# Performance work log

Hardware: AMD Instinct MI355X
Metric: run time of the kernel (lower is better)

## Reference

```python
import jax, jax.numpy as jnp
import numpy as np
from jax import lax

C = 31  # channels (hyperspectral bands)
DN = ('NCHW', 'OIHW', 'NCHW')


def ln_bias(x, w, b):
    # WithBias LayerNorm over channel dim (torch does it in (b,hw,c) layout)
    mu = x.mean(axis=1, keepdims=True)
    var = x.var(axis=1, keepdims=True)
    xn = (x - mu) * lax.rsqrt(var + 1e-5)
    return xn * w[None, :, None, None] + b[None, :, None, None]


def conv1x1(x, W, b):
    y = lax.conv_general_dilated(x, W, (1, 1), 'VALID', dimension_numbers=DN)
    return y + b[None, :, None, None]


def dwconv3(x, W, b=None):
    c = x.shape[1]
    y = lax.conv_general_dilated(x, W, (1, 1), ((1, 1), (1, 1)),
                                 dimension_numbers=DN, feature_group_count=c)
    if b is not None:
        y = y + b[None, :, None, None]
    return y


def l2norm_lastdim(v):
    n = jnp.sqrt(jnp.sum(v * v, axis=-1, keepdims=True))
    return v / jnp.maximum(n, 1e-12)


def setup_inputs() -> dict:
    key = jax.random.key(0)
    ks = jax.random.split(key, 16)
    B, H, W = 4, 512, 512
    s = 0.05
    d = {
        'x': jax.random.normal(ks[0], (B, 1, H, W), jnp.float32),
        'z': jax.random.normal(ks[1], (B, C, H, W), jnp.float32),
        'nx_w': jnp.ones((1,), jnp.float32),
        'nx_b': jnp.zeros((1,), jnp.float32),
        'nz_w': jnp.ones((C,), jnp.float32),
        'nz_b': jnp.zeros((C,), jnp.float32),
        't1_w': jax.random.normal(ks[2], (C, C, 1, 1), jnp.float32) * s,
        't1_b': jnp.zeros((C,), jnp.float32),
        't2_w': jax.random.normal(ks[3], (C, 1, 3, 3), jnp.float32) * s,
        't2_b': jnp.zeros((C,), jnp.float32),
        'p1_w': jax.random.normal(ks[4], (C, 1, 1, 1), jnp.float32) * s,
        'p1_b': jnp.zeros((C,), jnp.float32),
        'p2_w': jax.random.normal(ks[5], (C, 1, 3, 3), jnp.float32) * s,
        'p2_b': jnp.zeros((C,), jnp.float32),
        'g1_w': jax.random.normal(ks[6], (C, C, 1, 1), jnp.float32) * s,
        'g1_b': jnp.zeros((C,), jnp.float32),
        'g2_w': jax.random.normal(ks[7], (C, 1, 3, 3), jnp.float32) * s,
        'g2_b': jnp.zeros((C,), jnp.float32),
        'w_w': jax.random.normal(ks[8], (C, C, 1, 1), jnp.float32) * s,
        'w_b': jnp.zeros((C,), jnp.float32),
        'v_w': jax.random.normal(ks[9], (C + 1, C + 1, 1, 1), jnp.float32) * s,
        'v_b': jnp.zeros((C + 1,), jnp.float32),
        'pe1_w': jax.random.normal(ks[10], (C, 1, 3, 3), jnp.float32) * s,
        'pe2_w': jax.random.normal(ks[11], (C, 1, 3, 3), jnp.float32) * s,
    }
    return d


def reference(x, z, nx_w, nx_b, nz_w, nz_b, t1_w, t1_b, t2_w, t2_b,
              p1_w, p1_b, p2_w, p2_b, g1_w, g1_b, g2_w, g2_b,
              w_w, w_b, v_w, v_b, pe1_w, pe2_w):
    b, _, h, w = x.shape
    x0 = ln_bias(x, nx_w, nx_b)            # (b,1,h,w)
    z0 = ln_bias(z, nz_w, nz_b)            # (b,C,h,w)

    z1 = dwconv3(conv1x1(z0, t1_w, t1_b), t2_w, t2_b).reshape(b, C, h * w)
    x1 = dwconv3(conv1x1(x0, p1_w, p1_b), p2_w, p2_b).reshape(b, C, h * w)

    z1 = l2norm_lastdim(z1)
    x1 = l2norm_lastdim(x1)

    att = jax.nn.softmax(jnp.einsum('bcn,bdn->bcd', z1, x1), axis=-1)  # (b,C,C)

    z2 = dwconv3(conv1x1(z0, g1_w, g1_b), g2_w, g2_b)  # (b,C,h,w)
    z_v = z2.reshape(b, C, h * w)
    out_x = jnp.einsum('bcd,bdn->bcn', att, z_v).reshape(b, C, h, w)

    pos = dwconv3(jax.nn.gelu(dwconv3(z2, pe1_w), approximate=False), pe2_w)
    out_x = conv1x1(out_x, w_w, w_b) + pos + z

    y = conv1x1(jnp.concatenate([x, out_x], axis=1), v_w, v_b)  # (b,C+1,h,w)
    return y
```

## Files before the change

kernel.cpp:

```cpp
#include <hip/hip_runtime.h>
#include <hip/hip_fp16.h>
#include <math.h>

#define BN 4
#define CC 31
#define HH 512
#define WW 512
#define HWSZ 262144

static const size_t Z2F = (size_t)BN * CC * HWSZ;
#define T_OFF   0
#define SSQ_OFF 124
#define R0_OFF  248
#define RL_OFF  372
#define C0_OFF  496
#define CL_OFF  620
#define COR_OFF 744
#define M2_OFF  1240
#define VB2_OFF 5208

typedef short v8s __attribute__((ext_vector_type(8)));
typedef _Float16 v8h __attribute__((ext_vector_type(8)));
typedef float v4f __attribute__((ext_vector_type(4)));
typedef _Float16 v4h __attribute__((ext_vector_type(4)));

__device__ __forceinline__ short f2bf(float f) {
    unsigned u = __float_as_uint(f);
    return (short)((u + 0x7FFFu + ((u >> 16) & 1u)) >> 16);
}

__device__ __forceinline__ float fast_gelu(float s) {
    const float a  = fabsf(s) * 0.70710678118654752f;
    const float t  = __builtin_amdgcn_rcpf(1.f + 0.3275911f * a);
    float p = 1.061405429f;
    p = p * t - 1.453152027f;
    p = p * t + 1.421413741f;
    p = p * t - 0.284496736f;
    p = p * t + 0.254829592f;
    const float e  = __expf(-a * a);
    const float er = copysignf(1.f - p * t * e, s);
    return 0.5f * s * (1.f + er);
}

__device__ __forceinline__ void swizzle_tile(int& b, int& ty0, int& tx0) {
    const int lid = blockIdx.x + 32 * blockIdx.y + 1024 * blockIdx.z;
    const int vid = ((lid & 7) << 9) + (lid >> 3);
    b = vid >> 10;
    const int rem = vid & 1023;
    ty0 = (rem >> 5) << 4;
    tx0 = (rem & 31) << 4;
}

__global__ __launch_bounds__(256, 4) void blockNL_k_stage1(
    const float* __restrict__ z,
    const float* __restrict__ nz_w, const float* __restrict__ nz_b,
    const float* __restrict__ t1w, const float* __restrict__ t1b,
    const float* __restrict__ t2w, const float* __restrict__ t2b,
    const float* __restrict__ g1w, const float* __restrict__ g1b,
    const float* __restrict__ g2w, const float* __restrict__ g2b,
    __half* __restrict__ z2out, float* __restrict__ stats)
{
    __shared__ __align__(16) short Vb[324 * 32];
    __shared__ __align__(16) short Wp[16 * 32];
    __shared__ __align__(16) union {
        short Ff[324 * 16];
        short Zb[16 * 264];
    } uf;
    __shared__ __align__(16) short Wd[10 * 16];

    const int tid = threadIdx.x;
    int b, ty0, tx0;
    swizzle_tile(b, ty0, tx0);

    const int w = tid >> 6, lane = tid & 63, quad = lane >> 4, m15 = lane & 15;
    const int ty = tid >> 4, tx = tid & 15;
    const int gy = ty0 + ty, gx = tx0 + tx;

    for (int hp = tid; hp < 324; hp += 256) {
        const int hy = hp / 18, hx = hp - hy * 18;
        const int zy = ty0 + hy - 1, zx = tx0 + hx - 1;
        const bool valid = ((unsigned)zy < (unsigned)HH) && ((unsigned)zx < (unsigned)WW);
        int pk[16];
        if (valid) {
            const float* zp = z + (size_t)b * CC * HWSZ + (size_t)zy * WW + zx;
            float v[CC];
            float mu = 0.f;
            #pragma unroll
            for (int c = 0; c < CC; ++c) { v[c] = zp[(size_t)c * HWSZ]; mu += v[c]; }
            mu *= (1.f / 31.f);
            float var = 0.f;
            #pragma unroll
            for (int c = 0; c < CC; ++c) { float d = v[c] - mu; v[c] = d; var += d * d; }
            var *= (1.f / 31.f);
            const float rs = rsqrtf(var + 1e-5f);
            #pragma unroll
            for (int c = 0; c < CC; ++c) v[c] = v[c] * rs * nz_w[c] + nz_b[c];
            #pragma unroll
            for (int i = 0; i < 15; ++i)
                asm("v_cvt_pk_bf16_f32 %0, %1, %2"
                    : "=v"(pk[i]) : "v"(v[2 * i]), "v"(v[2 * i + 1]));
            asm("v_cvt_pk_bf16_f32 %0, %1, %2"
                : "=v"(pk[15]) : "v"(v[30]), "v"(0.f));
        } else {
            #pragma unroll
            for (int i = 0; i < 16; ++i) pk[i] = 0;
        }
        int* dst = (int*)&Vb[hp * 32];
        #pragma unroll
        for (int q = 0; q < 4; ++q) {
            int4 t; t.x = pk[q*4]; t.y = pk[q*4+1]; t.z = pk[q*4+2]; t.w = pk[q*4+3];
            ((int4*)dst)[q] = t;
        }
    }

    auto wbuild = [&](int p) {
        const float* W1 = (p >= 2) ? g1w : t1w;
        const int ct = p & 1;
        const int m = tid >> 4, kp = tid & 15;
        const int gr = ct * 16 + m;
        const int k0 = 2 * kp, k1 = k0 + 1;
        float w0 = 0.f, w1 = 0.f;
        if (gr < CC) {
            if (k0 < CC) w0 = W1[gr * CC + k0];
            if (k1 < CC) w1 = W1[gr * CC + k1];
        }
        ((int*)Wp)[m * 16 + kp] =
            (int)((unsigned short)f2bf(w0) | ((unsigned)(unsigned short)f2bf(w1) << 16));
    };

    auto wdbuild = [&](int p) {
        if (tid < 160) {
            const float* W3 = (p >= 2) ? g2w : t2w;
            const float* B3 = (p >= 2) ? g2b : t2b;
            const int tap = tid >> 4, r = tid & 15;
            const int ch = (p & 1) * 16 + r;
            float v = 0.f;
            if (ch < CC) v = (tap < 9) ? W3[ch * 9 + tap] : B3[ch];
            Wd[tap * 16 + r] = (short)__half_as_ushort(__float2half(v));
        }
    };

    auto mfma_pass = [&](int p) {
        const int ct = p & 1;
        const float* B1 = (p >= 2) ? g1b : t1b;
        const v8s afrag = *(const v8s*)&Wp[m15 * 32 + quad * 8];
        float bias[4];
        #pragma unroll
        for (int r = 0; r < 4; ++r) {
            const int row = ct * 16 + quad * 4 + r;
            bias[r] = (row < CC) ? B1[row] : 0.f;
        }
        for (int j = w; j < 21; j += 4) {
            const int px = j * 16 + m15;
            const int pc = (px < 324) ? px : 323;
            const v8s bfrag = *(const v8s*)&Vb[pc * 32 + quad * 8];
            v4f acc = {0.f, 0.f, 0.f, 0.f};
            acc = __builtin_amdgcn_mfma_f32_16x16x32_bf16(afrag, bfrag, acc, 0, 0, 0);
            if (px < 324) {
                unsigned d0 = (unsigned)__half_as_ushort(__float2half(acc[0] + bias[0]))
                            | ((unsigned)__half_as_ushort(__float2half(acc[1] + bias[1])) << 16);
                unsigned d1 = (unsigned)__half_as_ushort(__float2half(acc[2] + bias[2]))
                            | ((unsigned)__half_as_ushort(__float2half(acc[3] + bias[3])) << 16);
                const int half = (quad >> 1) ^ ((px >> 2) & 1);
                int2 st; st.x = (int)d0; st.y = (int)d1;
                *(int2*)&uf.Ff[px * 16 + half * 8 + (quad & 1) * 4] = st;
            }
        }
    };

    auto dw3_compute = [&](__half2* accv) {
        {
            const v8s b0 = *(const v8s*)&Wd[9 * 16 + 0];
            const v8s b1 = *(const v8s*)&Wd[9 * 16 + 8];
            #pragma unroll
            for (int i = 0; i < 4; ++i) {
                accv[i]     = ((const __half2*)&b0)[i];
                accv[4 + i] = ((const __half2*)&b1)[i];
            }
        }
        #pragma unroll
        for (int dy = 0; dy < 3; ++dy)
            #pragma unroll
            for (int dx = 0; dx < 3; ++dx) {
                const int tap = dy * 3 + dx;
                const int hp = (ty + dy) * 18 + (tx + dx);
                const int sel = (hp >> 2) & 1;
                const v8s f0 = *(const v8s*)&uf.Ff[hp * 16 + sel * 8];
                const v8s f1 = *(const v8s*)&uf.Ff[hp * 16 + (sel ^ 1) * 8];
                const v8s w0 = *(const v8s*)&Wd[tap * 16 + 0];
                const v8s w1 = *(const v8s*)&Wd[tap * 16 + 8];
                #pragma unroll
                for (int i = 0; i < 4; ++i) {
                    accv[i]     = __hfma2(((const __half2*)&w0)[i],
                                          ((const __half2*)&f0)[i], accv[i]);
                    accv[4 + i] = __hfma2(((const __half2*)&w1)[i],
                                          ((const __half2*)&f1)[i], accv[4 + i]);
                }
            }
    };

    auto dw3_writeT = [&](int ct, const __half2* accv) {
        #pragma unroll
        for (int i = 0; i < 8; ++i) {
            const unsigned u = *(const unsigned*)&accv[i];
            uf.Zb[(2 * i) * 264 + tid]     = (short)(u & 0xFFFFu);
            uf.Zb[(2 * i + 1) * 264 + tid] = (short)(u >> 16);
        }
        const bool top = (gy == 0), bot = (gy == HH - 1);
        const bool lef = (gx == 0), rig = (gx == WW - 1);
        if (top | bot | lef | rig) {
            #pragma unroll
            for (int r = 0; r < 16; ++r) {
                const int ch = ct * 16 + r;
                if (ch < CC) {
                    const unsigned u = *(const unsigned*)&accv[r >> 1];
                    const float sT = __half2float(__ushort_as_half(
                        (unsigned short)((r & 1) ? (u >> 16) : (u & 0xFFFFu))));
                    if (top) atomicAdd(&stats[R0_OFF + b * CC + ch], sT);
                    if (bot) atomicAdd(&stats[RL_OFF + b * CC + ch], sT);
                    if (lef) atomicAdd(&stats[C0_OFF + b * CC + ch], sT);
                    if (rig) atomicAdd(&stats[CL_OFF + b * CC + ch], sT);
                    if ((top || bot) && (lef || rig))
                        stats[COR_OFF + (b * CC + ch) * 4 +
                              (bot ? 2 : 0) + (rig ? 1 : 0)] = sT;
                }
            }
        }
    };

    auto dw3_writeG = [&](int ct, const __half2* accv) {
        const size_t zbase = (size_t)b * CC * HWSZ + (size_t)gy * WW + gx;
        #pragma unroll
        for (int i = 0; i < 8; ++i) {
            const unsigned u = *(const unsigned*)&accv[i];
            const int ch0 = ct * 16 + 2 * i, ch1 = ch0 + 1;
            z2out[zbase + (size_t)ch0 * HWSZ] =
                __ushort_as_half((unsigned short)(u & 0xFFFFu));
            if (ch1 < CC)
                z2out[zbase + (size_t)ch1 * HWSZ] =
                    __ushort_as_half((unsigned short)(u >> 16));
        }
    };

    auto stats_pass = [&](int ct) {
        const bool dosq = (w >> 1);
        const int kh = w & 1;
        v8h onesh;
        #pragma unroll
        for (int i = 0; i < 8; ++i) onesh[i] = (_Float16)1.f;
        v4f acc = {0.f, 0.f, 0.f, 0.f};
        #pragma unroll
        for (int i = 0; i < 4; ++i) {
            const int ks = kh * 4 + i;
            const v8h bf = *(const v8h*)&uf.Zb[m15 * 264 + ks * 32 + quad * 8];
            acc = __builtin_amdgcn_mfma_f32_16x16x32_f16(dosq ? bf : onesh, bf, acc, 0, 0, 0);
        }
        if (!dosq) {
            if (quad == 0) {
                const int ch = ct * 16 + m15;
                if (ch < CC) atomicAdd(&stats[T_OFF + b * CC + ch], acc[0]);
            }
        } else {
            if ((m15 >> 2) == quad) {
                const int r = m15 & 3;
                const int ch = ct * 16 + m15;
                if (ch < CC) atomicAdd(&stats[SSQ_OFF + b * CC + ch], acc[r]);
            }
        }
    };

    __half2 accv[8];

    wbuild(0); wdbuild(0);
    __syncthreads();
    mfma_pass(0);
    __syncthreads();
    dw3_compute(accv);
    __syncthreads();
    dw3_writeT(0, accv);
    __syncthreads();
    stats_pass(0); wbuild(1); wdbuild(1);
    __syncthreads();
    mfma_pass(1);
    __syncthreads();
    dw3_compute(accv);
    __syncthreads();
    dw3_writeT(1, accv);
    __syncthreads();
    stats_pass(1); wbuild(2); wdbuild(2);
    __syncthreads();
    mfma_pass(2);
    __syncthreads();
    dw3_compute(accv); dw3_writeG(2, accv); wbuild(3);
    __syncthreads();
    mfma_pass(3); wdbuild(3);
    __syncthreads();
    dw3_compute(accv); dw3_writeG(3, accv);
}

__global__ void blockNL_k_att(
    const float* __restrict__ nx_b,
    const float* __restrict__ p1w, const float* __restrict__ p1b,
    const float* __restrict__ p2w, const float* __restrict__ p2b,
    const float* __restrict__ ww,  const float* __restrict__ wb,
    const float* __restrict__ vw,  const float* __restrict__ vb,
    float* stats)
{
    __shared__ float x1v[CC][9];
    __shared__ float dxs[CC];
    __shared__ float att[CC][CC];
    __shared__ float WA[CC][CC];

    const int tid = threadIdx.x;
    const int b = blockIdx.x;
    const float cnt[9] = {1.f, 510.f, 1.f, 510.f, 260100.f, 510.f, 1.f, 510.f, 1.f};

    if (tid < CC) {
        const float a = nx_b[0];
        const float u = p1w[tid] * a + p1b[tid];
        float w9[9];
        #pragma unroll
        for (int k = 0; k < 9; ++k) w9[k] = p2w[tid * 9 + k];
        float ssq = 0.f;
        #pragma unroll
        for (int ry = 0; ry < 3; ++ry) {
            #pragma unroll
            for (int rx = 0; rx < 3; ++rx) {
                float wsum = 0.f;
                #pragma unroll
                for (int ky = 0; ky < 3; ++ky) {
                    #pragma unroll
                    for (int kx = 0; kx < 3; ++kx) {
                        const bool okr = (ry == 1) || (ry == 0 && ky >= 1) || (ry == 2 && ky <= 1);
                        const bool okc = (rx == 1) || (rx == 0 && kx >= 1) || (rx == 2 && kx <= 1);
                        if (okr && okc) wsum += w9[ky * 3 + kx];
                    }
                }
                const float val = u * wsum + p2b[tid];
                x1v[tid][ry * 3 + rx] = val;
                ssq += cnt[ry * 3 + rx] * val * val;
            }
        }
        dxs[tid] = fmaxf(sqrtf(ssq), 1e-12f);
    }
    if (b == 0 && tid < 32) {
        float s = vb[tid];
        #pragma unroll
        for (int c = 0; c < CC; ++c) s += vw[tid * 32 + c + 1] * wb[c];
        stats[VB2_OFF + tid] = s;
    }
    __syncthreads();

    if (tid < CC) {
        const int c = tid;
        const float Tt  = stats[T_OFF  + b * CC + c];
        const float sq  = stats[SSQ_OFF + b * CC + c];
        const float r0  = stats[R0_OFF + b * CC + c];
        const float rL  = stats[RL_OFF + b * CC + c];
        const float c0  = stats[C0_OFF + b * CC + c];
        const float cL  = stats[CL_OFF + b * CC + c];
        const float k00 = stats[COR_OFF + (b * CC + c) * 4 + 0];
        const float k01 = stats[COR_OFF + (b * CC + c) * 4 + 1];
        const float k10 = stats[COR_OFF + (b * CC + c) * 4 + 2];
        const float k11 = stats[COR_OFF + (b * CC + c) * 4 + 3];
        float T[9];
        T[0] = k00; T[2] = k01; T[6] = k10; T[8] = k11;
        T[1] = r0 - k00 - k01;
        T[7] = rL - k10 - k11;
        T[3] = c0 - k00 - k10;
        T[5] = cL - k01 - k11;
        T[4] = Tt - r0 - rL - c0 - cL + k00 + k01 + k10 + k11;
        const float dz = fmaxf(sqrtf(sq), 1e-12f);

        float Arow[CC];
        float mx = -3.4e38f;
        #pragma unroll
        for (int d = 0; d < CC; ++d) {
            float s = 0.f;
            #pragma unroll
            for (int r = 0; r < 9; ++r) s += T[r] * x1v[d][r];
            s = s / (dz * dxs[d]);
            Arow[d] = s;
            mx = fmaxf(mx, s);
        }
        float den = 0.f;
        #pragma unroll
        for (int d = 0; d < CC; ++d) { float e = expf(Arow[d] - mx); Arow[d] = e; den += e; }
        const float inv = 1.f / den;
        #pragma unroll
        for (int d = 0; d < CC; ++d) att[c][d] = Arow[d] * inv;
    }
    __syncthreads();
    if (tid < CC) {
        const int c2 = tid;
        #pragma unroll
        for (int d = 0; d < CC; ++d) {
            float s = 0.f;
            #pragma unroll
            for (int c = 0; c < CC; ++c) s += ww[c2 * CC + c] * att[c][d];
            WA[c2][d] = s;
        }
    }
    __syncthreads();
    if (tid < 32) {
        const int e = tid;
        #pragma unroll
        for (int d = 0; d < CC; ++d) {
            float s = 0.f;
            #pragma unroll
            for (int c2 = 0; c2 < CC; ++c2) s += vw[e * 32 + c2 + 1] * WA[c2][d];
            stats[M2_OFF + (b * 32 + e) * CC + d] = s;
        }
    }
}

__global__ __launch_bounds__(256, 4) void blockNL_k_out(
    const float* __restrict__ x, const float* __restrict__ z,
    const float* __restrict__ vw,
    const float* __restrict__ pe1w, const float* __restrict__ pe2w,
    const __half* __restrict__ z2, const float* __restrict__ stats,
    float* __restrict__ out)
{
    __shared__ __align__(16) unsigned zb2[4][400];
    __shared__ __align__(16) unsigned qb2[4][324];
    __shared__ __align__(16) short Ub[256 * 20];
    __shared__ __align__(16) short A2[4 * 32 * 20];
    __shared__ unsigned W1h[144];
    __shared__ unsigned W2h[144];

    const int tid = threadIdx.x;
    int b, ty0, tx0;
    swizzle_tile(b, ty0, tx0);
    const int ty = tid >> 4, tx = tid & 15;
    const int gy = ty0 + ty, gx = tx0 + tx;

    const float* M2 = stats + M2_OFF + b * 32 * CC;
    for (int idx = tid; idx < 2048; idx += 256) {
        const int ci = idx >> 9, e = (idx >> 4) & 31, k = idx & 15;
        const int ch = ci * 8 + (k & 7);
        float v = 0.f;
        if (ch < 31) v = (k < 8) ? vw[e * 32 + 1 + ch] : M2[e * CC + ch];
        A2[(ci * 32 + e) * 20 + k] = (short)__half_as_ushort(__float2half(v));
    }
    for (int idx = tid; idx < 288; idx += 256) {
        const int t = (idx >= 144);
        const int r = idx - t * 144;
        const int ci = r / 36, rem = r - ci * 36;
        const int tap = rem >> 2, pr = rem & 3;
        const int ch0 = ci * 8 + 2 * pr, ch1 = ch0 + 1;
        const float* Ws = t ? pe2w : pe1w;
        const float a = Ws[ch0 * 9 + tap];
        const float bb = (ch1 < 31) ? Ws[ch1 * 9 + tap] : 0.f;
        const unsigned u = (unsigned)__half_as_ushort(__float2half(a))
                         | ((unsigned)__half_as_ushort(__float2half(bb)) << 16);
        (t ? W2h : W1h)[r] = u;
    }

    const int w = tid >> 6, lane = tid & 63, quad = lane >> 4, m15 = lane & 15;
    const int mt = w & 1, jbase = (w >> 1) * 8;
    const size_t zpix = (size_t)b * CC * HWSZ + (size_t)gy * WW + gx;

    int  gzo[6];
    bool gvv[6];
    #pragma unroll
    for (int k = 0; k < 6; ++k) {
        const int p = lane + 64 * k;
        const int hy = p / 18, hx = p - hy * 18;
        const bool inr = (p < 324);
        gzo[k] = inr ? (hy * 20 + hx) : 0;
        gvv[k] = inr && ((unsigned)(ty0 + hy - 1) < (unsigned)HH) &&
                 ((unsigned)(tx0 + hx - 1) < (unsigned)WW);
    }
    const bool sact = (tid < 200);
    const int shy = tid / 10, shx2 = (tid - shy * 10) * 2;
    const int szy = ty0 + shy - 2, szx = tx0 + shx2 - 2;
    const bool sv = sact && ((unsigned)szy < (unsigned)HH) &&
                    ((unsigned)szx < (unsigned)WW);
    const long sgoff = (long)szy * WW + szx;
    const int zwo = shy * 20 + shx2;

    v4f acc[8];
    #pragma unroll
    for (int jj = 0; jj < 8; ++jj) acc[jj] = (v4f){0.f, 0.f, 0.f, 0.f};

    auto stage = [&](int ci) {
        const unsigned short* z2u = (const unsigned short*)z2;
        #pragma unroll
        for (int pr = 0; pr < 4; ++pr) {
            const int ch0 = ci * 8 + 2 * pr, ch1 = ch0 + 1;
            unsigned wa = 0, wb = 0;
            if (sv) {
                wa = *(const unsigned*)(z2u + (size_t)(b * CC + ch0) * HWSZ + sgoff);
                if (ch1 < 31)
                    wb = *(const unsigned*)(z2u + (size_t)(b * CC + ch1) * HWSZ + sgoff);
            }
            const unsigned u0 = (wa & 0xFFFFu) | (wb << 16);
            const unsigned u1 = (wa >> 16) | (wb & 0xFFFF0000u);
            if (sact) {
                uint2 st; st.x = u0; st.y = u1;
                *(uint2*)&zb2[pr][zwo] = st;
            }
        }
    };

    stage(0);

    for (int ci = 0; ci < 4; ++ci) {
        __syncthreads();
        {
            const int pr = w;
            unsigned wv2[9];
            #pragma unroll
            for (int t = 0; t < 9; ++t) wv2[t] = W1h[ci * 36 + t * 4 + pr];
            #pragma unroll
            for (int k = 0; k < 6; ++k) {
                const int p = lane + 64 * k;
                if (k < 5 || p < 324) {
                    unsigned qo = 0;
                    if (gvv[k]) {
                        __half2 s2h = __float2half2_rn(0.f);
                        #pragma unroll
                        for (int dy = 0; dy < 3; ++dy)
                            #pragma unroll
                            for (int dx = 0; dx < 3; ++dx)
                                s2h = __hfma2(*(const __half2*)&wv2[dy * 3 + dx],
                                              *(const __half2*)&zb2[pr][gzo[k] + dy * 20 + dx],
                                              s2h);
                        const float2 f = __half22float2(s2h);
                        const float q0 = fast_gelu(f.x), q1 = fast_gelu(f.y);
                        qo = (unsigned)__half_as_ushort(__float2half(q0))
                           | ((unsigned)__half_as_ushort(__float2half(q1)) << 16);
                    }
                    qb2[pr][p] = qo;
                }
            }
        }
        __syncthreads();
        {
            __half2 pos2[4];
            #pragma unroll
            for (int pr = 0; pr < 4; ++pr) pos2[pr] = __float2half2_rn(0.f);
            #pragma unroll
            for (int dy = 0; dy < 3; ++dy)
                #pragma unroll
                for (int dx = 0; dx < 3; ++dx) {
                    const int tap = dy * 3 + dx;
                    const int qoff = (ty + dy) * 18 + (tx + dx);
                    #pragma unroll
                    for (int pr = 0; pr < 4; ++pr) {
                        const unsigned wq = W2h[ci * 36 + tap * 4 + pr];
                        pos2[pr] = __hfma2(*(const __half2*)&wq,
                                           *(const __half2*)&qb2[pr][qoff], pos2[pr]);
                    }
                }
            unsigned tpk[4], zc[4];
            const int ctr = (ty + 2) * 20 + (tx + 2);
            #pragma unroll
            for (int pr = 0; pr < 4; ++pr) {
                zc[pr] = zb2[pr][ctr];
                const int ch0 = ci * 8 + 2 * pr, ch1 = ch0 + 1;
                const float2 pf = __half22float2(pos2[pr]);
                const float t0 = pf.x + z[zpix + (size_t)ch0 * HWSZ];
                float t1 = 0.f;
                if (ch1 < 31) t1 = pf.y + z[zpix + (size_t)ch1 * HWSZ];
                tpk[pr] = (unsigned)__half_as_ushort(__float2half(t0))
                        | ((unsigned)__half_as_ushort(__float2half(t1)) << 16);
            }
            int* ub = (int*)&Ub[tid * 20];
            int2 s0, s1, s2, s3;
            s0.x = (int)tpk[0]; s0.y = (int)tpk[1];
            s1.x = (int)tpk[2]; s1.y = (int)tpk[3];
            s2.x = (int)zc[0];  s2.y = (int)zc[1];
            s3.x = (int)zc[2];  s3.y = (int)zc[3];
            ((int2*)ub)[0] = s0;
            ((int2*)ub)[1] = s1;
            ((int2*)ub)[2] = s2;
            ((int2*)ub)[3] = s3;
        }
        __syncthreads();
        {
            const v4h a = *(const v4h*)&A2[(ci * 32 + mt * 16 + m15) * 20 + quad * 4];
            #pragma unroll
            for (int jj = 0; jj < 8; ++jj) {
                const int p = (jbase + jj) * 16 + m15;
                const v4h bv = *(const v4h*)&Ub[p * 20 + quad * 4];
                acc[jj] = __builtin_amdgcn_mfma_f32_16x16x16f16(a, bv, acc[jj], 0, 0, 0);
            }
        }
        if (ci < 3) stage(ci + 1);
    }

    {
        float vb2r[4], vw0[4];
        #pragma unroll
        for (int r = 0; r < 4; ++r) {
            const int e = mt * 16 + quad * 4 + r;
            vb2r[r] = stats[VB2_OFF + e];
            vw0[r]  = vw[e * 32];
        }
        #pragma unroll
        for (int jj = 0; jj < 8; ++jj) {
            const int p = (jbase + jj) * 16 + m15;
            const int py = p >> 4, px = p & 15;
            const int ogy = ty0 + py, ogx = tx0 + px;
            const float xv = x[(size_t)b * HWSZ + (size_t)ogy * WW + ogx];
            const size_t obase = (size_t)b * 32 * HWSZ + (size_t)ogy * WW + ogx;
            #pragma unroll
            for (int r = 0; r < 4; ++r) {
                const int e = mt * 16 + quad * 4 + r;
                out[obase + (size_t)e * HWSZ] = acc[jj][r] + vb2r[r] + vw0[r] * xv;
            }
        }
    }
}

extern "C" void kernel_launch(void* const* d_in, const int* in_sizes, int n_in,
                              void* d_out, int out_size, void* d_ws, size_t ws_size,
                              hipStream_t stream)
{
    (void)in_sizes; (void)n_in; (void)out_size; (void)ws_size;

    const float* x    = (const float*)d_in[0];
    const float* z    = (const float*)d_in[1];
    const float* nx_b = (const float*)d_in[3];
    const float* nz_w = (const float*)d_in[4];
    const float* nz_b = (const float*)d_in[5];
    const float* t1w  = (const float*)d_in[6];
    const float* t1b  = (const float*)d_in[7];
    const float* t2w  = (const float*)d_in[8];
    const float* t2b  = (const float*)d_in[9];
    const float* p1w  = (const float*)d_in[10];
    const float* p1b  = (const float*)d_in[11];
    const float* p2w  = (const float*)d_in[12];
    const float* p2b  = (const float*)d_in[13];
    const float* g1w  = (const float*)d_in[14];
    const float* g1b  = (const float*)d_in[15];
    const float* g2w  = (const float*)d_in[16];
    const float* g2b  = (const float*)d_in[17];
    const float* ww   = (const float*)d_in[18];
    const float* wb   = (const float*)d_in[19];
    const float* vw   = (const float*)d_in[20];
    const float* vb   = (const float*)d_in[21];
    const float* pe1w = (const float*)d_in[22];
    const float* pe2w = (const float*)d_in[23];

    __half* z2   = (__half*)d_ws;
    float* stats = (float*)((char*)d_ws + Z2F * sizeof(__half));

    hipMemsetAsync(stats, 0, 1240 * sizeof(float), stream);

    dim3 grid(WW / 16, HH / 16, BN);
    dim3 blk(256);

    blockNL_k_stage1<<<grid, blk, 0, stream>>>(z, nz_w, nz_b, t1w, t1b, t2w, t2b,
                                               g1w, g1b, g2w, g2b, z2, stats);
    blockNL_k_att<<<4, 64, 0, stream>>>(nx_b, p1w, p1b, p2w, p2b, ww, wb, vw, vb,
                                        stats);
    blockNL_k_out<<<grid, blk, 0, stream>>>(x, z, vw, pe1w, pe2w, z2, stats,
                                            (float*)d_out);
}
```

Measured before the change: 573.3 us.

## Fuse attention-matrix kernel into output kernel, recomputing per block

Removes the separate tiny attention kernel launch (4 blocks of 64 threads) by having every output block recompute the 31x31 softmax attention, the W·att and V·(W·att) products, and the bias fold from the global stats. The results go straight into the fp16 A2 MFMA operand in shared memory, and the shared buffers for this step are unioned with the halo buffers. This removes one kernel launch and the serialization bubble between kernels. In exchange, 4096 blocks each redo roughly 60K FMAs of small matrix work plus extra barriers, and the added registers may affect occupancy.

```diff
diff --git a/kernel.cpp b/kernel.cpp
--- a/kernel.cpp
+++ b/kernel.cpp
@@ -16,8 +16,6 @@
 #define C0_OFF  496
 #define CL_OFF  620
 #define COR_OFF 744
-#define M2_OFF  1240
-#define VB2_OFF 5208
 
 typedef short v8s __attribute__((ext_vector_type(8)));
 typedef _Float16 v8h __attribute__((ext_vector_type(8)));
@@ -298,59 +296,100 @@
     dw3_compute(accv); dw3_writeG(3, accv);
 }
 
-__global__ void blockNL_k_att(
+__global__ __launch_bounds__(256, 4) void blockNL_k_out(
+    const float* __restrict__ x, const float* __restrict__ z,
     const float* __restrict__ nx_b,
     const float* __restrict__ p1w, const float* __restrict__ p1b,
     const float* __restrict__ p2w, const float* __restrict__ p2b,
     const float* __restrict__ ww,  const float* __restrict__ wb,
     const float* __restrict__ vw,  const float* __restrict__ vb,
-    float* stats)
+    const float* __restrict__ pe1w, const float* __restrict__ pe2w,
+    const __half* __restrict__ z2, const float* __restrict__ stats,
+    float* __restrict__ out)
 {
-    __shared__ float x1v[CC][9];
-    __shared__ float dxs[CC];
-    __shared__ float att[CC][CC];
-    __shared__ float WA[CC][CC];
+    __shared__ __align__(16) union {
+        struct {
+            unsigned zb2[4][400];
+            unsigned qb2[4][324];
+        } s;
+        struct {
+            float x1v[CC][9];
+            float dxs[CC];
+            float att[CC][CC];
+            float WA[CC][CC];
+        } a;
+    } uu;
+    __shared__ __align__(16) short Ub[256 * 20];
+    __shared__ __align__(16) short A2[4 * 32 * 20];
+    __shared__ unsigned W1h[144];
+    __shared__ unsigned W2h[144];
+    __shared__ float vb2s[32];
 
     const int tid = threadIdx.x;
-    const int b = blockIdx.x;
-    const float cnt[9] = {1.f, 510.f, 1.f, 510.f, 260100.f, 510.f, 1.f, 510.f, 1.f};
-
-    if (tid < CC) {
-        const float a = nx_b[0];
-        const float u = p1w[tid] * a + p1b[tid];
-        float w9[9];
-        #pragma unroll
-        for (int k = 0; k < 9; ++k) w9[k] = p2w[tid * 9 + k];
-        float ssq = 0.f;
-        #pragma unroll
-        for (int ry = 0; ry < 3; ++ry) {
-            #pragma unroll
-            for (int rx = 0; rx < 3; ++rx) {
-                float wsum = 0.f;
+    int b, ty0, tx0;
+    swizzle_tile(b, ty0, tx0);
+    const int ty = tid >> 4, tx = tid & 15;
+    const int gy = ty0 + ty, gx = tx0 + tx;
+
+    {
+        const float cnt[9] = {1.f, 510.f, 1.f, 510.f, 260100.f, 510.f, 1.f, 510.f, 1.f};
+        if (tid < CC) {
+            const float a = nx_b[0];
+            const float u = p1w[tid] * a + p1b[tid];
+            float w9[9];
+            #pragma unroll
+            for (int k = 0; k < 9; ++k) w9[k] = p2w[tid * 9 + k];
+            float ssq = 0.f;
+            #pragma unroll
+            for (int ry = 0; ry < 3; ++ry) {
                 #pragma unroll
-                for (int ky = 0; ky < 3; ++ky) {
+                for (int rx = 0; rx < 3; ++rx) {
+                    float wsum = 0.f;
                     #pragma unroll
-                    for (int kx = 0; kx < 3; ++kx) {
-                        const bool okr = (ry == 1) || (ry == 0 && ky >= 1) || (ry == 2 && ky <= 1);
-                        const bool okc = (rx == 1) || (rx == 0 && kx >= 1) || (rx == 2 && kx <= 1);
-                        if (okr && okc) wsum += w9[ky * 3 + kx];
+                    for (int ky = 0; ky < 3; ++ky) {
+                        #pragma unroll
+                        for (int kx = 0; kx < 3; ++kx) {
+                            const bool okr = (ry == 1) || (ry == 0 && ky >= 1) || (ry == 2 && ky <= 1);
+                            const bool okc = (rx == 1) || (rx == 0 && kx >= 1) || (rx == 2 && kx <= 1);
+                            if (okr && okc) wsum += w9[ky * 3 + kx];
+                        }
                     }
+                    const float val = u * wsum + p2b[tid];
+                    uu.a.x1v[tid][ry * 3 + rx] = val;
+                    ssq += cnt[ry * 3 + rx] * val * val;
                 }
-                const float val = u * wsum + p2b[tid];
-                x1v[tid][ry * 3 + rx] = val;
-                ssq += cnt[ry * 3 + rx] * val * val;
-            }
-        }
-        dxs[tid] = fmaxf(sqrtf(ssq), 1e-12f);
-    }
-    if (b == 0 && tid < 32) {
-        float s = vb[tid];
-        #pragma unroll
-        for (int c = 0; c < CC; ++c) s += vw[tid * 32 + c + 1] * wb[c];
-        stats[VB2_OFF + tid] = s;
-    }
-    __syncthreads();
-
+            }
+            uu.a.dxs[tid] = fmaxf(sqrtf(ssq), 1e-12f);
+        }
+        if (tid >= 64 && tid < 96) {
+            const int e = tid - 64;
+            float s = vb[e];
+            #pragma unroll
+            for (int c = 0; c < CC; ++c) s += vw[e * 32 + c + 1] * wb[c];
+            vb2s[e] = s;
+        }
+    }
+    for (int idx = tid; idx < 2048; idx += 256) {
+        const int ci = idx >> 9, e = (idx >> 4) & 31, k = idx & 15;
+        const int ch = ci * 8 + (k & 7);
+        float v = 0.f;
+        if (k < 8 && ch < 31) v = vw[e * 32 + 1 + ch];
+        A2[(ci * 32 + e) * 20 + k] = (short)__half_as_ushort(__float2half(v));
+    }
+    for (int idx = tid; idx < 288; idx += 256) {
+        const int t = (idx >= 144);
+        const int r = idx - t * 144;
+        const int ci = r / 36, rem = r - ci * 36;
+        const int tap = rem >> 2, pr = rem & 3;
+        const int ch0 = ci * 8 + 2 * pr, ch1 = ch0 + 1;
+        const float* Ws = t ? pe2w : pe1w;
+        const float a = Ws[ch0 * 9 + tap];
+        const float bb = (ch1 < 31) ? Ws[ch1 * 9 + tap] : 0.f;
+        const unsigned u = (unsigned)__half_as_ushort(__float2half(a))
+                         | ((unsigned)__half_as_ushort(__float2half(bb)) << 16);
+        (t ? W2h : W1h)[r] = u;
+    }
+    __syncthreads();
     if (tid < CC) {
         const int c = tid;
         const float Tt  = stats[T_OFF  + b * CC + c];
@@ -378,83 +417,36 @@
         for (int d = 0; d < CC; ++d) {
             float s = 0.f;
             #pragma unroll
-            for (int r = 0; r < 9; ++r) s += T[r] * x1v[d][r];
-            s = s / (dz * dxs[d]);
+            for (int r = 0; r < 9; ++r) s += T[r] * uu.a.x1v[d][r];
+            s = s / (dz * uu.a.dxs[d]);
             Arow[d] = s;
             mx = fmaxf(mx, s);
         }
         float den = 0.f;
         #pragma unroll
-        for (int d = 0; d < CC; ++d) { float e = expf(Arow[d] - mx); Arow[d] = e; den += e; }
+        for (int d = 0; d < CC; ++d) { float e = __expf(Arow[d] - mx); Arow[d] = e; den += e; }
         const float inv = 1.f / den;
         #pragma unroll
-        for (int d = 0; d < CC; ++d) att[c][d] = Arow[d] * inv;
-    }
-    __syncthreads();
-    if (tid < CC) {
-        const int c2 = tid;
-        #pragma unroll
-        for (int d = 0; d < CC; ++d) {
-            float s = 0.f;
-            #pragma unroll
-            for (int c = 0; c < CC; ++c) s += ww[c2 * CC + c] * att[c][d];
-            WA[c2][d] = s;
-        }
-    }
-    __syncthreads();
-    if (tid < 32) {
-        const int e = tid;
-        #pragma unroll
-        for (int d = 0; d < CC; ++d) {
-            float s = 0.f;
-            #pragma unroll
-            for (int c2 = 0; c2 < CC; ++c2) s += vw[e * 32 + c2 + 1] * WA[c2][d];
-            stats[M2_OFF + (b * 32 + e) * CC + d] = s;
-        }
-    }
-}
-
-__global__ __launch_bounds__(256, 4) void blockNL_k_out(
-    const float* __restrict__ x, const float* __restrict__ z,
-    const float* __restrict__ vw,
-    const float* __restrict__ pe1w, const float* __restrict__ pe2w,
-    const __half* __restrict__ z2, const float* __restrict__ stats,
-    float* __restrict__ out)
-{
-    __shared__ __align__(16) unsigned zb2[4][400];
-    __shared__ __align__(16) unsigned qb2[4][324];
-    __shared__ __align__(16) short Ub[256 * 20];
-    __shared__ __align__(16) short A2[4 * 32 * 20];
-    __shared__ unsigned W1h[144];
-    __shared__ unsigned W2h[144];
-
-    const int tid = threadIdx.x;
-    int b, ty0, tx0;
-    swizzle_tile(b, ty0, tx0);
-    const int ty = tid >> 4, tx = tid & 15;
-    const int gy = ty0 + ty, gx = tx0 + tx;
-
-    const float* M2 = stats + M2_OFF + b * 32 * CC;
-    for (int idx = tid; idx < 2048; idx += 256) {
-        const int ci = idx >> 9, e = (idx >> 4) & 31, k = idx & 15;
-        const int ch = ci * 8 + (k & 7);
-        float v = 0.f;
-        if (ch < 31) v = (k < 8) ? vw[e * 32 + 1 + ch] : M2[e * CC + ch];
-        A2[(ci * 32 + e) * 20 + k] = (short)__half_as_ushort(__float2half(v));
-    }
-    for (int idx = tid; idx < 288; idx += 256) {
-        const int t = (idx >= 144);
-        const int r = idx - t * 144;
-        const int ci = r / 36, rem = r - ci * 36;
-        const int tap = rem >> 2, pr = rem & 3;
-        const int ch0 = ci * 8 + 2 * pr, ch1 = ch0 + 1;
-        const float* Ws = t ? pe2w : pe1w;
-        const float a = Ws[ch0 * 9 + tap];
-        const float bb = (ch1 < 31) ? Ws[ch1 * 9 + tap] : 0.f;
-        const unsigned u = (unsigned)__half_as_ushort(__float2half(a))
-                         | ((unsigned)__half_as_ushort(__float2half(bb)) << 16);
-        (t ? W2h : W1h)[r] = u;
-    }
+        for (int d = 0; d < CC; ++d) uu.a.att[c][d] = Arow[d] * inv;
+    }
+    __syncthreads();
+    for (int idx = tid; idx < CC * CC; idx += 256) {
+        const int c2 = idx / CC, d = idx - c2 * CC;
+        float s = 0.f;
+        #pragma unroll
+        for (int c = 0; c < CC; ++c) s += ww[c2 * CC + c] * uu.a.att[c][d];
+        uu.a.WA[c2][d] = s;
+    }
+    __syncthreads();
+    for (int idx = tid; idx < 32 * CC; idx += 256) {
+        const int e = idx / CC, d = idx - e * CC;
+        float s = 0.f;
+        #pragma unroll
+        for (int c2 = 0; c2 < CC; ++c2) s += vw[e * 32 + c2 + 1] * uu.a.WA[c2][d];
+        A2[((d >> 3) * 32 + e) * 20 + 8 + (d & 7)] =
+            (short)__half_as_ushort(__float2half(s));
+    }
+    __syncthreads();
 
     const int w = tid >> 6, lane = tid & 63, quad = lane >> 4, m15 = lane & 15;
     const int mt = w & 1, jbase = (w >> 1) * 8;
@@ -488,17 +480,17 @@
         #pragma unroll
         for (int pr = 0; pr < 4; ++pr) {
             const int ch0 = ci * 8 + 2 * pr, ch1 = ch0 + 1;
-            unsigned wa = 0, wb = 0;
+            unsigned wa = 0, wb2 = 0;
             if (sv) {
                 wa = *(const unsigned*)(z2u + (size_t)(b * CC + ch0) * HWSZ + sgoff);
                 if (ch1 < 31)
-                    wb = *(const unsigned*)(z2u + (size_t)(b * CC + ch1) * HWSZ + sgoff);
-            }
-            const unsigned u0 = (wa & 0xFFFFu) | (wb << 16);
-            const unsigned u1 = (wa >> 16) | (wb & 0xFFFF0000u);
+                    wb2 = *(const unsigned*)(z2u + (size_t)(b * CC + ch1) * HWSZ + sgoff);
+            }
+            const unsigned u0 = (wa & 0xFFFFu) | (wb2 << 16);
+            const unsigned u1 = (wa >> 16) | (wb2 & 0xFFFF0000u);
             if (sact) {
                 uint2 st; st.x = u0; st.y = u1;
-                *(uint2*)&zb2[pr][zwo] = st;
+                *(uint2*)&uu.s.zb2[pr][zwo] = st;
             }
         }
     };
@@ -524,14 +516,14 @@
                             #pragma unroll
                             for (int dx = 0; dx < 3; ++dx)
                                 s2h = __hfma2(*(const __half2*)&wv2[dy * 3 + dx],
-                                              *(const __half2*)&zb2[pr][gzo[k] + dy * 20 + dx],
+                                              *(const __half2*)&uu.s.zb2[pr][gzo[k] + dy * 20 + dx],
                                               s2h);
                         const float2 f = __half22float2(s2h);
                         const float q0 = fast_gelu(f.x), q1 = fast_gelu(f.y);
                         qo = (unsigned)__half_as_ushort(__float2half(q0))
                            | ((unsigned)__half_as_ushort(__float2half(q1)) << 16);
                     }
-                    qb2[pr][p] = qo;
+                    uu.s.qb2[pr][p] = qo;
                 }
             }
         }
@@ -550,14 +542,14 @@
                     for (int pr = 0; pr < 4; ++pr) {
                         const unsigned wq = W2h[ci * 36 + tap * 4 + pr];
                         pos2[pr] = __hfma2(*(const __half2*)&wq,
-                                           *(const __half2*)&qb2[pr][qoff], pos2[pr]);
+                                           *(const __half2*)&uu.s.qb2[pr][qoff], pos2[pr]);
                     }
                 }
             unsigned tpk[4], zc[4];
             const int ctr = (ty + 2) * 20 + (tx + 2);
             #pragma unroll
             for (int pr = 0; pr < 4; ++pr) {
-                zc[pr] = zb2[pr][ctr];
+                zc[pr] = uu.s.zb2[pr][ctr];
                 const int ch0 = ci * 8 + 2 * pr, ch1 = ch0 + 1;
                 const float2 pf = __half22float2(pos2[pr]);
                 const float t0 = pf.x + z[zpix + (size_t)ch0 * HWSZ];
@@ -595,7 +587,7 @@
         #pragma unroll
         for (int r = 0; r < 4; ++r) {
             const int e = mt * 16 + quad * 4 + r;
-            vb2r[r] = stats[VB2_OFF + e];
+            vb2r[r] = vb2s[e];
             vw0[r]  = vw[e * 32];
         }
         #pragma unroll
@@ -654,8 +646,7 @@
 
     blockNL_k_stage1<<<grid, blk, 0, stream>>>(z, nz_w, nz_b, t1w, t1b, t2w, t2b,
                                                g1w, g1b, g2w, g2b, z2, stats);
-    blockNL_k_att<<<4, 64, 0, stream>>>(nx_b, p1w, p1b, p2w, p2b, ww, wb, vw, vb,
-                                        stats);
-    blockNL_k_out<<<grid, blk, 0, stream>>>(x, z, vw, pe1w, pe2w, z2, stats,
-                                            (float*)d_out);
+    blockNL_k_out<<<grid, blk, 0, stream>>>(x, z, nx_b, p1w, p1b, p2w, p2b,
+                                            ww, wb, vw, vb, pe1w, pe2w,
+                                            z2, stats, (float*)d_out);
 }
```

Result: faster. 529.0 us (-7.7%).
